# Kernel optimization log

Measured on AMD Instinct MI355X. Metric: run time of the kernel, lower is better.

Reference implementation:

```python
import jax, jax.numpy as jnp
import numpy as np

N_USERS = 100000
N_ITEMS = 50000
DIM = 64
N_EDGES = 4_000_000
NUM_LAYERS = 3


def setup_inputs() -> dict:
    key = jax.random.key(0)
    k1, k2, k3 = jax.random.split(key, 3)
    # xavier_uniform-like scale for embeddings
    scale = float(np.sqrt(6.0 / (N_USERS + DIM)))
    user_emb = jax.random.uniform(k1, (N_USERS, DIM), jnp.float32, -scale, scale)
    scale_i = float(np.sqrt(6.0 / (N_ITEMS + DIM)))
    item_emb = jax.random.uniform(k2, (N_ITEMS, DIM), jnp.float32, -scale_i, scale_i)
    edge_index = jax.random.randint(k3, (2, N_EDGES), 0, N_USERS + N_ITEMS, dtype=jnp.int64)
    return {"user_emb": user_emb, "item_emb": item_emb, "edge_index": edge_index}


def reference(user_emb, item_emb, edge_index):
    """LightGCN_W.encode_window: K rounds of symmetric-normalized SpMM, then layer mean."""
    n_users = user_emb.shape[0]
    n_nodes = n_users + item_emb.shape[0]
    row, col = edge_index[0], edge_index[1]  # messages flow row (source) -> col (target)

    # gcn_norm with add_self_loops=False (PyG LGConv default)
    ones = jnp.ones(row.shape[0], dtype=user_emb.dtype)
    deg = jax.ops.segment_sum(ones, col, num_segments=n_nodes)
    dinv = jnp.where(deg > 0, jax.lax.rsqrt(jnp.maximum(deg, 1e-12)), 0.0)
    norm = (dinv[row] * dinv[col])[:, None]  # [E, 1]

    x = jnp.concatenate([user_emb, item_emb], axis=0)  # [N, D]
    acc = x
    for _ in range(NUM_LAYERS):
        x = jax.ops.segment_sum(norm * x[row], col, num_segments=n_nodes)
        acc = acc + x
    out = acc / (NUM_LAYERS + 1)
    return out[:n_users], out[n_users:]
```

## Files before the change

### kernel.cpp

```cpp
#include <hip/hip_runtime.h>
#include <hip/hip_fp16.h>

#define DIM 64
#define BSH 8
#define BMASK 255u
#define NBMAX 1024
#define BINC 16384
#define BSTRIDE 8192


__global__ void zero_ints(int* __restrict__ p, int n) {
    int i = blockIdx.x * blockDim.x + threadIdx.x;
    if (i < n) p[i] = 0;
}

__global__ __launch_bounds__(1024) void bin_kernel(const int* __restrict__ edge, int E,
                                                   int* __restrict__ bcur,
                                                   unsigned* __restrict__ bin, int NB) {
    __shared__ unsigned stage[BINC];
    __shared__ int lcnt[NBMAX];
    __shared__ int lsc[NBMAX];
    __shared__ int lcur[NBMAX];
    __shared__ int gb[NBMAX];
    const int tid = (int)threadIdx.x;
    const int beg = (int)blockIdx.x * BINC;
    const int n = min(BINC, E - beg);

    lcnt[tid] = 0;
    __syncthreads();
    for (int i = tid; i < n; i += 1024)
        atomicAdd(&lcnt[edge[E + beg + i] >> BSH], 1);
    __syncthreads();
    lsc[tid] = lcnt[tid];
    __syncthreads();
    for (int off = 1; off < 1024; off <<= 1) {
        int t = (tid >= off) ? lsc[tid - off] : 0;
        __syncthreads();
        lsc[tid] += t;
        __syncthreads();
    }
    {
        int cb = lcnt[tid];
        lcur[tid] = lsc[tid] - cb;
        if (tid < NB) gb[tid] = cb ? atomicAdd(&bcur[tid], cb) : 0;
    }
    __syncthreads();
    for (int i = tid; i < n; i += 1024) {
        int r = edge[beg + i];
        int c = edge[E + beg + i];
        int b = c >> BSH;
        int slot = atomicAdd(&lcur[b], 1);
        stage[slot] = ((unsigned)r << BSH) | ((unsigned)c & BMASK);
    }
    __syncthreads();
    const int wid = tid >> 6, lane = tid & 63;
    for (int b = wid; b < NB; b += 16) {
        int cb = lcnt[b];
        if (!cb) continue;
        int lb = lsc[b] - cb;
        int g = b * BSTRIDE + gb[b];
        for (int l = lane; l < cb; l += 64)
            bin[g + l] = stage[lb + l];
    }
}

__global__ __launch_bounds__(256) void csr_kernel(const unsigned* __restrict__ bin,
                                                  const int* __restrict__ bcnt,
                                                  const float* __restrict__ user,
                                                  const float* __restrict__ item,
                                                  int nU,
                                                  int2* __restrict__ pdesc,
                                                  float* __restrict__ dinv,
                                                  float* __restrict__ rdinv,
                                                  int* __restrict__ row_sorted,
                                                  __half* __restrict__ y0,
                                                  int nN) {
    __shared__ unsigned sbin[BSTRIDE];
    __shared__ int lcnt[256];
    __shared__ int lsc[256];
    __shared__ int lcur[256];
    __shared__ float sdinv[256];
    const int tid = (int)threadIdx.x;
    const int b = (int)blockIdx.x;
    const int abase = b * BSTRIDE;
    const int cnt = bcnt[b];
    lcnt[tid] = 0;
    for (int i = tid; i < cnt; i += 256)
        sbin[i] = bin[abase + i];
    __syncthreads();
    for (int i = tid; i < cnt; i += 256)
        atomicAdd(&lcnt[sbin[i] & BMASK], 1);
    __syncthreads();
    lsc[tid] = lcnt[tid];
    __syncthreads();
    for (int off = 1; off < 256; off <<= 1) {
        int t = (tid >= off) ? lsc[tid - off] : 0;
        __syncthreads();
        lsc[tid] += t;
        __syncthreads();
    }
    const int cb = lcnt[tid];
    const int lb = lsc[tid] - cb;
    lcur[tid] = abase + lb;
    float dv = cb ? rsqrtf((float)cb) : 0.0f;
    sdinv[tid] = dv;
    int node = (b << BSH) + tid;
    if (node < nN) {
        pdesc[node] = make_int2(abase + lb, cb);
        dinv[node] = dv;
        rdinv[node] = cb ? sqrtf((float)cb) : 0.0f;
    }
    __syncthreads();
    for (int i = tid; i < cnt; i += 256) {
        unsigned e = sbin[i];
        int c = (int)(e & BMASK);
        int p = atomicAdd(&lcur[c], 1);
        row_sorted[p] = (int)(e >> BSH);
    }
    const int baseNode = b << BSH;
#pragma unroll
    for (int it = 0; it < 8; ++it) {
        int idx = it * 256 + tid;
        int ln = idx >> 3;
        int node2 = baseNode + ln;
        if (node2 < nN) {
            int qc = idx & 7;
            const float* src = (node2 < nU) ? user + (size_t)node2 * DIM
                                            : item + (size_t)(node2 - nU) * DIM;
            float4 e0 = ((const float4*)src)[qc * 2];
            float4 e1 = ((const float4*)src)[qc * 2 + 1];
            float dvn = sdinv[ln];
            float4 pack;
            __half2* p = (__half2*)&pack;
            p[0] = __floats2half2_rn(dvn * e0.x, dvn * e0.y);
            p[1] = __floats2half2_rn(dvn * e0.z, dvn * e0.w);
            p[2] = __floats2half2_rn(dvn * e1.x, dvn * e1.y);
            p[3] = __floats2half2_rn(dvn * e1.z, dvn * e1.w);
            ((float4*)y0)[(size_t)baseNode * 8 + idx] = pack;
        }
    }
}

__global__ void zero_row_kernel(__half* __restrict__ r1, __half* __restrict__ r2,
                                __half* __restrict__ r3, int nN) {
    int t = threadIdx.x;
    size_t o = (size_t)nN * DIM + t;
    r1[o] = __float2half(0.0f);
    r2[o] = __float2half(0.0f);
    r3[o] = __float2half(0.0f);
}

template<bool LAST>
__global__ __launch_bounds__(256) void layer_kernel(const int2* __restrict__ pdesc,
                                                    const float* __restrict__ dinv,
                                                    const int* __restrict__ row_sorted,
                                                    const __half* __restrict__ y_in,
                                                    __half* __restrict__ y_out,
                                                    const float* __restrict__ user,
                                                    const float* __restrict__ item,
                                                    const float* __restrict__ rdinv,
                                                    const __half* __restrict__ y_prev,
                                                    float* __restrict__ out,
                                                    int nU, int nN) {
    int wave = (int)((blockIdx.x * blockDim.x + threadIdx.x) >> 6);
    int lane = (int)(threadIdx.x & 63);
    if (wave >= nN) return;
    const int2 pd = pdesc[wave];
    const int beg = pd.x;
    const int n = pd.y;
    const int zrow = nN;
    const int g = lane >> 3;
    const int q = lane & 7;
    const float4* yv = (const float4*)y_in;
    __half2 acc0 = __float2half2_rn(0.0f);
    __half2 acc1 = acc0, acc2 = acc0, acc3 = acc0;
    for (int base = 0; base < n; base += 32) {
        int s = base + g;
        int e = beg + s;
        int i0 = (s      < n) ? row_sorted[e]      : zrow;
        int i1 = (s + 8  < n) ? row_sorted[e + 8]  : zrow;
        int i2 = (s + 16 < n) ? row_sorted[e + 16] : zrow;
        int i3 = (s + 24 < n) ? row_sorted[e + 24] : zrow;
        float4 v0 = yv[(size_t)i0 * 8 + q];
        float4 v1 = yv[(size_t)i1 * 8 + q];
        float4 v2 = yv[(size_t)i2 * 8 + q];
        float4 v3 = yv[(size_t)i3 * 8 + q];
        const __half2* h0 = (const __half2*)&v0;
        const __half2* h1 = (const __half2*)&v1;
        const __half2* h2 = (const __half2*)&v2;
        const __half2* h3 = (const __half2*)&v3;
        acc0 = __hadd2(acc0, h0[0]); acc1 = __hadd2(acc1, h0[1]);
        acc2 = __hadd2(acc2, h0[2]); acc3 = __hadd2(acc3, h0[3]);
        acc0 = __hadd2(acc0, h1[0]); acc1 = __hadd2(acc1, h1[1]);
        acc2 = __hadd2(acc2, h1[2]); acc3 = __hadd2(acc3, h1[3]);
        acc0 = __hadd2(acc0, h2[0]); acc1 = __hadd2(acc1, h2[1]);
        acc2 = __hadd2(acc2, h2[2]); acc3 = __hadd2(acc3, h2[3]);
        acc0 = __hadd2(acc0, h3[0]); acc1 = __hadd2(acc1, h3[1]);
        acc2 = __hadd2(acc2, h3[2]); acc3 = __hadd2(acc3, h3[3]);
    }
#pragma unroll
    for (int ofs = 8; ofs <= 32; ofs <<= 1) {
        int t0 = __shfl_xor(*reinterpret_cast<int*>(&acc0), ofs);
        int t1 = __shfl_xor(*reinterpret_cast<int*>(&acc1), ofs);
        int t2 = __shfl_xor(*reinterpret_cast<int*>(&acc2), ofs);
        int t3 = __shfl_xor(*reinterpret_cast<int*>(&acc3), ofs);
        acc0 = __hadd2(acc0, *reinterpret_cast<__half2*>(&t0));
        acc1 = __hadd2(acc1, *reinterpret_cast<__half2*>(&t1));
        acc2 = __hadd2(acc2, *reinterpret_cast<__half2*>(&t2));
        acc3 = __hadd2(acc3, *reinterpret_cast<__half2*>(&t3));
    }
    if (g == 0) {
        float dc = dinv[wave];
        float2 s0 = __half22float2(acc0);
        float2 s1 = __half22float2(acc1);
        float2 s2 = __half22float2(acc2);
        float2 s3 = __half22float2(acc3);
        if (!LAST) {
            float s = dc * dc;
            float4 pack;
            __half2* ph = (__half2*)&pack;
            ph[0] = __floats2half2_rn(s * s0.x, s * s0.y);
            ph[1] = __floats2half2_rn(s * s1.x, s * s1.y);
            ph[2] = __floats2half2_rn(s * s2.x, s * s2.y);
            ph[3] = __floats2half2_rn(s * s3.x, s * s3.y);
            ((float4*)y_out)[(size_t)wave * 8 + q] = pack;
        } else {
            float rd = rdinv[wave];
            float4 y1r = ((const float4*)y_prev)[(size_t)wave * 8 + q];
            float4 y2r = ((const float4*)y_in)[(size_t)wave * 8 + q];
            const __half2* p1 = (const __half2*)&y1r;
            const __half2* p2 = (const __half2*)&y2r;
            float w[8];
#pragma unroll
            for (int j = 0; j < 4; ++j) {
                float2 u1 = __half22float2(p1[j]);
                float2 u2 = __half22float2(p2[j]);
                w[2 * j]     = u1.x + u2.x;
                w[2 * j + 1] = u1.y + u2.y;
            }
            const float* src = (wave < nU) ? user + (size_t)wave * DIM
                                           : item + (size_t)(wave - nU) * DIM;
            float4 e0 = ((const float4*)src)[q * 2];
            float4 e1 = ((const float4*)src)[q * 2 + 1];
            float4 o0, o1;
            o0.x = 0.25f * (e0.x + rd * w[0] + dc * s0.x);
            o0.y = 0.25f * (e0.y + rd * w[1] + dc * s0.y);
            o0.z = 0.25f * (e0.z + rd * w[2] + dc * s1.x);
            o0.w = 0.25f * (e0.w + rd * w[3] + dc * s1.y);
            o1.x = 0.25f * (e1.x + rd * w[4] + dc * s2.x);
            o1.y = 0.25f * (e1.y + rd * w[5] + dc * s2.y);
            o1.z = 0.25f * (e1.z + rd * w[6] + dc * s3.x);
            o1.w = 0.25f * (e1.w + rd * w[7] + dc * s3.y);
            float4* o4 = (float4*)(out + (size_t)wave * DIM + q * 8);
            o4[0] = o0;
            o4[1] = o1;
        }
    }
}


extern "C" void kernel_launch(void* const* d_in, const int* in_sizes, int n_in,
                              void* d_out, int out_size, void* d_ws, size_t ws_size,
                              hipStream_t stream) {
    const float* user = (const float*)d_in[0];
    const float* item = (const float*)d_in[1];
    const int*   edge = (const int*)d_in[2];

    const int nU = in_sizes[0] / DIM;
    const int nI = in_sizes[1] / DIM;
    const int nN = nU + nI;
    const int E  = in_sizes[2] / 2;
    const int NB = (nN + 255) / 256;

    float* out = (float*)d_out;

    char* ws = (char*)d_ws;
    size_t off = 0;
    auto take = [&](size_t bytes) -> char* {
        char* p = ws + off;
        off = (off + bytes + 255) & ~(size_t)255;
        return p;
    };
    const size_t ytab = (size_t)(nN + 1) * DIM * 2;
    const size_t arena = (size_t)NB * BSTRIDE * 4;
    int*      bcur       = (int*)  take((size_t)NB * 4);
    int2*     pdesc      = (int2*) take((size_t)nN * 8);
    float*    dinv       = (float*)take((size_t)nN * 4);
    float*    rdinv      = (float*)take((size_t)nN * 4);
    int*      row_sorted = (int*)  take(arena);
    char*     R1 = take(arena > ytab ? arena : ytab);
    char*     R2 = take(ytab);
    char*     R3 = take(ytab);
    unsigned* bin = (unsigned*)R1;
    __half*   y1  = (__half*)R1;
    __half*   y0  = (__half*)R2;
    __half*   y2  = (__half*)R3;
    (void)ws_size; (void)n_in; (void)out_size;

    const int B = 256;
    dim3 blk(B);

    zero_ints<<<dim3((NB + B - 1) / B), blk, 0, stream>>>(bcur, NB);
    bin_kernel<<<dim3((E + BINC - 1) / BINC), dim3(1024), 0, stream>>>(edge, E, bcur, bin, NB);
    csr_kernel<<<dim3(NB), blk, 0, stream>>>(bin, bcur, user, item, nU,
                                             pdesc, dinv, rdinv, row_sorted, y0, nN);
    zero_row_kernel<<<dim3(1), dim3(64), 0, stream>>>(y0, y1, y2, nN);

    dim3 lgrid((nN + 3) / 4);
    layer_kernel<false><<<lgrid, blk, 0, stream>>>(pdesc, dinv, row_sorted, y0, y1,
                                                   nullptr, nullptr, nullptr, nullptr, nullptr,
                                                   nU, nN);
    layer_kernel<false><<<lgrid, blk, 0, stream>>>(pdesc, dinv, row_sorted, y1, y2,
                                                   nullptr, nullptr, nullptr, nullptr, nullptr,
                                                   nU, nN);
    layer_kernel<true ><<<lgrid, blk, 0, stream>>>(pdesc, dinv, row_sorted, y2, nullptr,
                                                   user, item, rdinv, y1, out,
                                                   nU, nN);
}
```

Measured before the change: 281.6 us.

## Pack node descriptors into float4, stage edges in LDS, reuse fp16 y0 for embeddings

```diff
diff --git a/kernel.cpp b/kernel.cpp
--- a/kernel.cpp
+++ b/kernel.cpp
@@ -5,7 +5,7 @@
 #define BSH 8
 #define BMASK 255u
 #define NBMAX 1024
-#define BINC 16384
+#define BINC 12288
 #define BSTRIDE 8192
 
 
@@ -17,6 +17,8 @@
 __global__ __launch_bounds__(1024) void bin_kernel(const int* __restrict__ edge, int E,
                                                    int* __restrict__ bcur,
                                                    unsigned* __restrict__ bin, int NB) {
+    __shared__ unsigned ent[BINC];
+    __shared__ unsigned short bkt[BINC];
     __shared__ unsigned stage[BINC];
     __shared__ int lcnt[NBMAX];
     __shared__ int lsc[NBMAX];
@@ -28,8 +30,14 @@
 
     lcnt[tid] = 0;
     __syncthreads();
-    for (int i = tid; i < n; i += 1024)
-        atomicAdd(&lcnt[edge[E + beg + i] >> BSH], 1);
+    for (int i = tid; i < n; i += 1024) {
+        int r = edge[beg + i];
+        int c = edge[E + beg + i];
+        int b = c >> BSH;
+        ent[i] = ((unsigned)r << BSH) | ((unsigned)c & BMASK);
+        bkt[i] = (unsigned short)b;
+        atomicAdd(&lcnt[b], 1);
+    }
     __syncthreads();
     lsc[tid] = lcnt[tid];
     __syncthreads();
@@ -46,11 +54,9 @@
     }
     __syncthreads();
     for (int i = tid; i < n; i += 1024) {
-        int r = edge[beg + i];
-        int c = edge[E + beg + i];
-        int b = c >> BSH;
+        int b = (int)bkt[i];
         int slot = atomicAdd(&lcur[b], 1);
-        stage[slot] = ((unsigned)r << BSH) | ((unsigned)c & BMASK);
+        stage[slot] = ent[i];
     }
     __syncthreads();
     const int wid = tid >> 6, lane = tid & 63;
@@ -69,9 +75,7 @@
                                                   const float* __restrict__ user,
                                                   const float* __restrict__ item,
                                                   int nU,
-                                                  int2* __restrict__ pdesc,
-                                                  float* __restrict__ dinv,
-                                                  float* __restrict__ rdinv,
+                                                  float4* __restrict__ pdesc,
                                                   int* __restrict__ row_sorted,
                                                   __half* __restrict__ y0,
                                                   int nN) {
@@ -106,9 +110,12 @@
     sdinv[tid] = dv;
     int node = (b << BSH) + tid;
     if (node < nN) {
-        pdesc[node] = make_int2(abase + lb, cb);
-        dinv[node] = dv;
-        rdinv[node] = cb ? sqrtf((float)cb) : 0.0f;
+        float4 pd;
+        pd.x = __int_as_float(abase + lb);
+        pd.y = __int_as_float(cb);
+        pd.z = dv;
+        pd.w = cb ? sqrtf((float)cb) : 0.0f;
+        pdesc[node] = pd;
     }
     __syncthreads();
     for (int i = tid; i < cnt; i += 256) {
@@ -151,23 +158,24 @@
 }
 
 template<bool LAST>
-__global__ __launch_bounds__(256) void layer_kernel(const int2* __restrict__ pdesc,
-                                                    const float* __restrict__ dinv,
+__global__ __launch_bounds__(256) void layer_kernel(const float4* __restrict__ pdesc,
                                                     const int* __restrict__ row_sorted,
                                                     const __half* __restrict__ y_in,
                                                     __half* __restrict__ y_out,
                                                     const float* __restrict__ user,
                                                     const float* __restrict__ item,
-                                                    const float* __restrict__ rdinv,
+                                                    const __half* __restrict__ y_zero,
                                                     const __half* __restrict__ y_prev,
                                                     float* __restrict__ out,
                                                     int nU, int nN) {
     int wave = (int)((blockIdx.x * blockDim.x + threadIdx.x) >> 6);
     int lane = (int)(threadIdx.x & 63);
     if (wave >= nN) return;
-    const int2 pd = pdesc[wave];
-    const int beg = pd.x;
-    const int n = pd.y;
+    const float4 pd = pdesc[wave];
+    const int beg = __float_as_int(pd.x);
+    const int n = __float_as_int(pd.y);
+    const float dc = pd.z;
+    const float rd = pd.w;
     const int zrow = nN;
     const int g = lane >> 3;
     const int q = lane & 7;
@@ -210,7 +218,6 @@
         acc3 = __hadd2(acc3, *reinterpret_cast<__half2*>(&t3));
     }
     if (g == 0) {
-        float dc = dinv[wave];
         float2 s0 = __half22float2(acc0);
         float2 s1 = __half22float2(acc1);
         float2 s2 = __half22float2(acc2);
@@ -225,7 +232,6 @@
             ph[3] = __floats2half2_rn(s * s3.x, s * s3.y);
             ((float4*)y_out)[(size_t)wave * 8 + q] = pack;
         } else {
-            float rd = rdinv[wave];
             float4 y1r = ((const float4*)y_prev)[(size_t)wave * 8 + q];
             float4 y2r = ((const float4*)y_in)[(size_t)wave * 8 + q];
             const __half2* p1 = (const __half2*)&y1r;
@@ -238,19 +244,33 @@
                 w[2 * j]     = u1.x + u2.x;
                 w[2 * j + 1] = u1.y + u2.y;
             }
-            const float* src = (wave < nU) ? user + (size_t)wave * DIM
-                                           : item + (size_t)(wave - nU) * DIM;
-            float4 e0 = ((const float4*)src)[q * 2];
-            float4 e1 = ((const float4*)src)[q * 2 + 1];
+            float emb[8];
+            if (rd != 0.0f) {
+                float4 y0r = ((const float4*)y_zero)[(size_t)wave * 8 + q];
+                const __half2* p0 = (const __half2*)&y0r;
+#pragma unroll
+                for (int j = 0; j < 4; ++j) {
+                    float2 u0 = __half22float2(p0[j]);
+                    emb[2 * j]     = rd * u0.x;
+                    emb[2 * j + 1] = rd * u0.y;
+                }
+            } else {
+                const float* src = (wave < nU) ? user + (size_t)wave * DIM
+                                               : item + (size_t)(wave - nU) * DIM;
+                float4 e0 = ((const float4*)src)[q * 2];
+                float4 e1 = ((const float4*)src)[q * 2 + 1];
+                emb[0] = e0.x; emb[1] = e0.y; emb[2] = e0.z; emb[3] = e0.w;
+                emb[4] = e1.x; emb[5] = e1.y; emb[6] = e1.z; emb[7] = e1.w;
+            }
             float4 o0, o1;
-            o0.x = 0.25f * (e0.x + rd * w[0] + dc * s0.x);
-            o0.y = 0.25f * (e0.y + rd * w[1] + dc * s0.y);
-            o0.z = 0.25f * (e0.z + rd * w[2] + dc * s1.x);
-            o0.w = 0.25f * (e0.w + rd * w[3] + dc * s1.y);
-            o1.x = 0.25f * (e1.x + rd * w[4] + dc * s2.x);
-            o1.y = 0.25f * (e1.y + rd * w[5] + dc * s2.y);
-            o1.z = 0.25f * (e1.z + rd * w[6] + dc * s3.x);
-            o1.w = 0.25f * (e1.w + rd * w[7] + dc * s3.y);
+            o0.x = 0.25f * (emb[0] + rd * w[0] + dc * s0.x);
+            o0.y = 0.25f * (emb[1] + rd * w[1] + dc * s0.y);
+            o0.z = 0.25f * (emb[2] + rd * w[2] + dc * s1.x);
+            o0.w = 0.25f * (emb[3] + rd * w[3] + dc * s1.y);
+            o1.x = 0.25f * (emb[4] + rd * w[4] + dc * s2.x);
+            o1.y = 0.25f * (emb[5] + rd * w[5] + dc * s2.y);
+            o1.z = 0.25f * (emb[6] + rd * w[6] + dc * s3.x);
+            o1.w = 0.25f * (emb[7] + rd * w[7] + dc * s3.y);
             float4* o4 = (float4*)(out + (size_t)wave * DIM + q * 8);
             o4[0] = o0;
             o4[1] = o1;
@@ -283,11 +303,9 @@
     };
     const size_t ytab = (size_t)(nN + 1) * DIM * 2;
     const size_t arena = (size_t)NB * BSTRIDE * 4;
-    int*      bcur       = (int*)  take((size_t)NB * 4);
-    int2*     pdesc      = (int2*) take((size_t)nN * 8);
-    float*    dinv       = (float*)take((size_t)nN * 4);
-    float*    rdinv      = (float*)take((size_t)nN * 4);
-    int*      row_sorted = (int*)  take(arena);
+    int*      bcur       = (int*)   take((size_t)NB * 4);
+    float4*   pdesc      = (float4*)take((size_t)nN * 16);
+    int*      row_sorted = (int*)   take(arena);
     char*     R1 = take(arena > ytab ? arena : ytab);
     char*     R2 = take(ytab);
     char*     R3 = take(ytab);
@@ -303,17 +321,17 @@
     zero_ints<<<dim3((NB + B - 1) / B), blk, 0, stream>>>(bcur, NB);
     bin_kernel<<<dim3((E + BINC - 1) / BINC), dim3(1024), 0, stream>>>(edge, E, bcur, bin, NB);
     csr_kernel<<<dim3(NB), blk, 0, stream>>>(bin, bcur, user, item, nU,
-                                             pdesc, dinv, rdinv, row_sorted, y0, nN);
+                                             pdesc, row_sorted, y0, nN);
     zero_row_kernel<<<dim3(1), dim3(64), 0, stream>>>(y0, y1, y2, nN);
 
     dim3 lgrid((nN + 3) / 4);
-    layer_kernel<false><<<lgrid, blk, 0, stream>>>(pdesc, dinv, row_sorted, y0, y1,
+    layer_kernel<false><<<lgrid, blk, 0, stream>>>(pdesc, row_sorted, y0, y1,
                                                    nullptr, nullptr, nullptr, nullptr, nullptr,
                                                    nU, nN);
-    layer_kernel<false><<<lgrid, blk, 0, stream>>>(pdesc, dinv, row_sorted, y1, y2,
+    layer_kernel<false><<<lgrid, blk, 0, stream>>>(pdesc, row_sorted, y1, y2,
                                                    nullptr, nullptr, nullptr, nullptr, nullptr,
                                                    nU, nN);
-    layer_kernel<true ><<<lgrid, blk, 0, stream>>>(pdesc, dinv, row_sorted, y2, nullptr,
-                                                   user, item, rdinv, y1, out,
+    layer_kernel<true ><<<lgrid, blk, 0, stream>>>(pdesc, row_sorted, y2, nullptr,
+                                                   user, item, y0, y1, out,
                                                    nU, nN);
 }
```

Result: no change. 286.2 us (+1.6%).
